# Optimization experiments

Measured on AMD Instinct MI355X. Metric: run time of the kernel, lower is better.

Reference implementation:

```python
import jax, jax.numpy as jnp
import numpy as np

HEADS, DIM_HEAD, DIM = 8, 64, 512
INNER = HEADS * DIM_HEAD  # 512


def setup_inputs() -> dict:
    key = jax.random.key(0)
    k1, k2, k3 = jax.random.split(key, 3)
    b, n = 2, 2048
    x = jax.random.normal(k1, (b, n, DIM), dtype=jnp.float32)
    # to_qkv: Linear(dim, 4*inner_dim, bias=False); weight stored [out, in]
    w_qkv = jax.random.normal(k2, (4 * INNER, DIM), dtype=jnp.float32) * (1.0 / np.sqrt(DIM))
    # to_out: Linear(2*inner_dim, dim) with bias
    w_out = jax.random.normal(k3, (DIM, 2 * INNER), dtype=jnp.float32) * (1.0 / np.sqrt(2 * INNER))
    b_out = jnp.zeros((DIM,), dtype=jnp.float32)
    return {"x": x, "w_qkv": w_qkv, "w_out": w_out, "b_out": b_out}


def reference(x, w_qkv, w_out, b_out):
    b, n, d = x.shape
    qkvt = x @ w_qkv.T  # [b, n, 4*inner]
    q, k, v, t = jnp.split(qkvt, 4, axis=-1)

    def split_heads(z):
        return z.reshape(b, n, HEADS, DIM_HEAD).transpose(0, 2, 1, 3)  # [b,h,n,dh]

    q, k, v, t = map(split_heads, (q, k, v, t))

    scale = DIM_HEAD ** -0.5
    dots = jnp.einsum('bhid,bhjd->bhij', q, k) * scale
    attn1 = jax.nn.softmax(dots, axis=-1)

    # fixed positional-decay attention: exp(-|i-j|/e), torch broadcast-normalized
    idx = jnp.arange(1, n + 1, dtype=x.dtype)  # linspace(1, n, n)
    tg = jnp.abs(idx[None, :] - idx[:, None])  # [n, n]
    a2 = jnp.exp(-tg / jnp.exp(jnp.asarray(1.0, x.dtype)))
    a2 = a2 / a2.sum(-1)  # broadcasts over last axis, as in the torch code

    out1 = jnp.einsum('bhij,bhjd->bhid', attn1, v)
    out2 = jnp.einsum('ij,bhjd->bhid', a2, t)
    out = jnp.concatenate([out1, out2], axis=-1)  # [b,h,n,2*dh]
    out = out.transpose(0, 2, 1, 3).reshape(b, n, HEADS * 2 * DIM_HEAD)  # [b,n,2*inner]
    return out @ w_out.T + b_out
```

## Files before the change

### kernel.cpp

```cpp
#include <hip/hip_runtime.h>
#include <hip/hip_bf16.h>
#include <stdint.h>

typedef unsigned short u16;
typedef __bf16 bf16;
typedef __bf16 bf16x8 __attribute__((ext_vector_type(8)));
typedef float f32x4 __attribute__((ext_vector_type(4)));
typedef float f32x16 __attribute__((ext_vector_type(16)));

#define NSEQ 2048
#define NDH 64
#define NH 8
#define QKS 2097152ull

__device__ __forceinline__ float b2f(u16 u) {
  union { float f; uint32_t i; } x; x.i = ((uint32_t)u) << 16; return x.f;
}
__device__ __forceinline__ u16 f2b(float f) {
  union { float f; uint32_t i; } x; x.f = f;
  const uint32_t r = x.i + 0x7FFFu + ((x.i >> 16) & 1u);
  return (u16)(r >> 16);
}
__device__ __forceinline__ uint32_t b2pk(float a, float b) {
  union { __hip_bfloat162 h; uint32_t u; } x;
  x.h = __float22bfloat162_rn(make_float2(a, b));
  return x.u;
}

__global__ __launch_bounds__(256) void k_gemm_qkvt(
    const float* __restrict__ X, const float* __restrict__ W, u16* __restrict__ qkvt) {
  __shared__ __align__(16) bf16 smem[18432];
  bf16* As = smem;
  bf16* Bs = smem + 5120;
  const int tid = threadIdx.x;
  const int n0 = blockIdx.x * 128;
  const int m0 = blockIdx.y * 128;
  const int w = tid >> 6, lane = tid & 63;
  const int wy = w >> 1, wx = w & 1;
  const int quad = lane >> 4, l15 = lane & 15;
  const int srow = tid >> 1, shalf = (tid & 1) * 16;
  const float* ax = X + (size_t)(m0 + srow) * 512 + shalf;
  const float* bx = W + (size_t)(n0 + srow) * 512 + shalf;
  f32x4 acc[4][4];
#pragma unroll
  for (int mt = 0; mt < 4; ++mt)
#pragma unroll
    for (int nt = 0; nt < 4; ++nt) acc[mt][nt] = (f32x4){0.f, 0.f, 0.f, 0.f};
  float4 af[4], bf4[4];
#pragma unroll
  for (int p = 0; p < 4; ++p) {
    af[p]  = *(const float4*)(ax + p * 4);
    bf4[p] = *(const float4*)(bx + p * 4);
  }
  for (int kc = 0; kc < 512; kc += 32) {
    __syncthreads();
    {
      uint4 ta = {b2pk(af[0].x, af[0].y), b2pk(af[0].z, af[0].w),
                  b2pk(af[1].x, af[1].y), b2pk(af[1].z, af[1].w)};
      uint4 tb = {b2pk(af[2].x, af[2].y), b2pk(af[2].z, af[2].w),
                  b2pk(af[3].x, af[3].y), b2pk(af[3].z, af[3].w)};
      *(uint4*)&As[srow * 40 + shalf]     = ta;
      *(uint4*)&As[srow * 40 + shalf + 8] = tb;
      uint4 tc = {b2pk(bf4[0].x, bf4[0].y), b2pk(bf4[0].z, bf4[0].w),
                  b2pk(bf4[1].x, bf4[1].y), b2pk(bf4[1].z, bf4[1].w)};
      uint4 td = {b2pk(bf4[2].x, bf4[2].y), b2pk(bf4[2].z, bf4[2].w),
                  b2pk(bf4[3].x, bf4[3].y), b2pk(bf4[3].z, bf4[3].w)};
      *(uint4*)&Bs[srow * 40 + shalf]     = tc;
      *(uint4*)&Bs[srow * 40 + shalf + 8] = td;
    }
    __syncthreads();
    if (kc + 32 < 512) {
#pragma unroll
      for (int p = 0; p < 4; ++p) {
        af[p]  = *(const float4*)(ax + kc + 32 + p * 4);
        bf4[p] = *(const float4*)(bx + kc + 32 + p * 4);
      }
    }
    bf16x8 afr[4], bfr[4];
#pragma unroll
    for (int mt = 0; mt < 4; ++mt)
      afr[mt] = *(const bf16x8*)&As[(wy * 64 + mt * 16 + l15) * 40 + quad * 8];
#pragma unroll
    for (int nt = 0; nt < 4; ++nt)
      bfr[nt] = *(const bf16x8*)&Bs[(wx * 64 + nt * 16 + l15) * 40 + quad * 8];
#pragma unroll
    for (int mt = 0; mt < 4; ++mt)
#pragma unroll
      for (int nt = 0; nt < 4; ++nt)
        acc[mt][nt] = __builtin_amdgcn_mfma_f32_16x16x32_bf16(afr[mt], bfr[nt], acc[mt][nt], 0, 0, 0);
  }
  __syncthreads();
  const int cbase = n0 + wx * 64;
  const int which = cbase >> 9;
  const int h     = (cbase >> 6) & 7;
  const float scale = (which == 0) ? 0.18033688011112043f : 1.0f;
  bf16* Cw = smem + w * 4608;
  if (which == 2) {
#pragma unroll
    for (int nt = 0; nt < 4; ++nt)
#pragma unroll
      for (int mt = 0; mt < 4; ++mt)
#pragma unroll
        for (int r = 0; r < 4; ++r)
          Cw[(nt * 16 + l15) * 72 + mt * 16 + quad * 4 + r] = (bf16)acc[mt][nt][r];
  } else {
#pragma unroll
    for (int mt = 0; mt < 4; ++mt)
#pragma unroll
      for (int nt = 0; nt < 4; ++nt)
#pragma unroll
        for (int r = 0; r < 4; ++r)
          Cw[(mt * 16 + quad * 4 + r) * 72 + nt * 16 + l15] = (bf16)(acc[mt][nt][r] * scale);
  }
  const int mb = m0 + wy * 64;
  const int bb = mb >> 11;
  const int nn0 = mb & (NSEQ - 1);
  if (which == 2) {
    u16* vt = qkvt + 2ull * QKS + (size_t)(bb * NH + h) * NDH * NSEQ;
#pragma unroll
    for (int p = 0; p < 8; ++p) {
      const int d = p * 8 + (lane >> 3);
      const int t8 = (lane & 7) * 8;
      const uint4 v = *(const uint4*)&Cw[d * 72 + t8];
      *(uint4*)(vt + (size_t)d * NSEQ + nn0 + t8) = v;
    }
  } else {
    u16* dst = qkvt + (size_t)which * QKS + ((size_t)(bb * NH + h) * NSEQ + nn0) * NDH;
#pragma unroll
    for (int p = 0; p < 8; ++p) {
      const int tok = p * 8 + (lane >> 3);
      const int c8 = (lane & 7) * 8;
      const uint4 v = *(const uint4*)&Cw[tok * 72 + c8];
      *(uint4*)(dst + (size_t)tok * NDH + c8) = v;
    }
  }
}

__global__ __launch_bounds__(256) void k_attn(
    const u16* __restrict__ qkvt, u16* __restrict__ out12) {
  __shared__ __align__(16) bf16 Qs[64 * 72];
  __shared__ __align__(16) bf16 KV[2 * 64 * 72];
  __shared__ __align__(16) bf16 Pw[4 * 32 * 72];
  __shared__ float Lpart[4][32];
  bf16* Ks = KV;
  bf16* Vt = KV + 64 * 72;
  const int tid = threadIdx.x;
  const int bh  = blockIdx.x;
  const int q0  = blockIdx.y * 64;
  const size_t base  = (size_t)bh * (NSEQ * NDH);
  const size_t vbase = 2ull * QKS + (size_t)bh * (NDH * NSEQ);
  const int wq = tid >> 6, lane = tid & 63;
  const int qh = wq >> 1, kh = wq & 1;
  const int l31 = lane & 31, hi = lane >> 5;
  const int srow = tid >> 2, sc0 = (tid & 3) * 16;
  {
    const u16* qp = qkvt + base + (size_t)(q0 + srow) * NDH + sc0;
    *(uint4*)&Qs[srow * 72 + sc0]     = *(const uint4*)qp;
    *(uint4*)&Qs[srow * 72 + sc0 + 8] = *(const uint4*)(qp + 8);
  }
  __syncthreads();
  bf16x8 qb[4];
#pragma unroll
  for (int c = 0; c < 4; ++c)
    qb[c] = *(const bf16x8*)&Qs[(qh * 32 + l31) * 72 + c * 16 + hi * 8];
  float lacc = 0.f;
  f32x16 o[2];
#pragma unroll
  for (int nt = 0; nt < 2; ++nt)
#pragma unroll
    for (int r = 0; r < 16; ++r) o[nt][r] = 0.f;
  const u16* kp = qkvt + QKS + base + (size_t)srow * NDH + sc0;
  const u16* vp = qkvt + vbase + (size_t)srow * NSEQ + sc0;
  uint4 k0 = *(const uint4*)kp;
  uint4 k1 = *(const uint4*)(kp + 8);
  uint4 v0 = *(const uint4*)vp;
  uint4 v1 = *(const uint4*)(vp + 8);
  for (int kt = 0; kt < 32; ++kt) {
    __syncthreads();
    *(uint4*)&Ks[srow * 72 + sc0]     = k0;
    *(uint4*)&Ks[srow * 72 + sc0 + 8] = k1;
    *(uint4*)&Vt[srow * 72 + sc0]     = v0;
    *(uint4*)&Vt[srow * 72 + sc0 + 8] = v1;
    __syncthreads();
    if (kt < 31) {
      const u16* kn = kp + (size_t)(kt + 1) * 64 * NDH;
      const u16* vn = vp + (kt + 1) * 64;
      k0 = *(const uint4*)kn;
      k1 = *(const uint4*)(kn + 8);
      v0 = *(const uint4*)vn;
      v1 = *(const uint4*)(vn + 8);
    }
    f32x16 s;
#pragma unroll
    for (int r = 0; r < 16; ++r) s[r] = 0.f;
#pragma unroll
    for (int c = 0; c < 4; ++c) {
      const bf16x8 ka = *(const bf16x8*)&Ks[(kh * 32 + l31) * 72 + c * 16 + hi * 8];
      s = __builtin_amdgcn_mfma_f32_32x32x16_bf16(ka, qb[c], s, 0, 0, 0);
    }
    float ts = 0.f;
#pragma unroll
    for (int r = 0; r < 16; ++r) {
      s[r] = __builtin_amdgcn_exp2f(s[r]);
      ts += s[r];
    }
    ts += __shfl_xor(ts, 32);
    lacc += ts;
    bf16* pr = Pw + (wq * 32 + l31) * 72;
#pragma unroll
    for (int g = 0; g < 4; ++g) {
      bf16 pk[4] = {(bf16)s[4 * g], (bf16)s[4 * g + 1],
                    (bf16)s[4 * g + 2], (bf16)s[4 * g + 3]};
      *(uint2*)&pr[g * 8 + hi * 4] = *(const uint2*)pk;
    }
#pragma unroll
    for (int c = 0; c < 2; ++c) {
      const bf16x8 pa = *(const bf16x8*)&Pw[(wq * 32 + l31) * 72 + c * 16 + hi * 8];
      const bf16x8 vb0 = *(const bf16x8*)&Vt[l31 * 72 + kh * 32 + c * 16 + hi * 8];
      const bf16x8 vb1 = *(const bf16x8*)&Vt[(32 + l31) * 72 + kh * 32 + c * 16 + hi * 8];
      o[0] = __builtin_amdgcn_mfma_f32_32x32x16_bf16(pa, vb0, o[0], 0, 0, 0);
      o[1] = __builtin_amdgcn_mfma_f32_32x32x16_bf16(pa, vb1, o[1], 0, 0, 0);
    }
  }
  __syncthreads();
  if (lane < 32) Lpart[wq][lane] = lacc;
  float* Osum = (float*)KV;
  if (kh == 1) {
#pragma unroll
    for (int nt = 0; nt < 2; ++nt)
#pragma unroll
      for (int r = 0; r < 16; ++r) {
        const int row = (r & 3) + 8 * (r >> 2) + 4 * hi;
        Osum[(qh * 32 + row) * 64 + nt * 32 + l31] = o[nt][r];
      }
  }
  __syncthreads();
  if (kh == 0) {
    const int bb = bh >> 3, h = bh & 7;
#pragma unroll
    for (int r = 0; r < 16; ++r) {
      const int row = (r & 3) + 8 * (r >> 2) + 4 * hi;
      const float lt = Lpart[qh * 2][row] + Lpart[qh * 2 + 1][row];
      const float inv = 1.f / lt;
      const int nn = q0 + qh * 32 + row;
      u16* dst = out12 + (size_t)(bb * NSEQ + nn) * 1024 + h * 128;
      dst[l31]      = f2b((o[0][r] + Osum[(qh * 32 + row) * 64 + l31]) * inv);
      dst[32 + l31] = f2b((o[1][r] + Osum[(qh * 32 + row) * 64 + 32 + l31]) * inv);
    }
  }
}

__global__ __launch_bounds__(256) void k_band(
    const u16* __restrict__ qkvt, u16* __restrict__ out12) {
  __shared__ float sinv[4][192];
  __shared__ float fbuf[4][64][68];
  const int tid = threadIdx.x;
  const int w = tid >> 6, d = tid & 63;
  const int c  = blockIdx.x * 4 + w;
  const int i0 = c * 64;
  const int bh = blockIdx.y;
  const size_t tb = 3ull * QKS + (size_t)bh * (NSEQ * NDH);
  const float EI = 0.36787944117144233f;
  const float RR = 0.69220062755534635f;
  const float OMR = 1.f - RR;
#pragma unroll
  for (int p = 0; p < 3; ++p) {
    const int j = i0 - 64 + p * 64 + d;
    const float r1 = __expf(-(float)(j + 1) * EI);
    const float r2 = __expf(-(float)(NSEQ - j) * EI);
    sinv[w][p * 64 + d] = OMR / (1.f - r1 + RR - r2);
  }
  const u16* tp = qkvt + tb + d;
  float f = 0.f;
  if (c > 0) {
#pragma unroll 8
    for (int jj = 0; jj < 64; ++jj)
      f = RR * f + sinv[w][jj] * b2f(tp[(size_t)(i0 - 64 + jj) * NDH]);
  }
#pragma unroll 8
  for (int jj = 0; jj < 64; ++jj) {
    f = RR * f + sinv[w][64 + jj] * b2f(tp[(size_t)(i0 + jj) * NDH]);
    fbuf[w][jj][d] = f;
  }
  float b = 0.f;
  if (c < 31) {
#pragma unroll 8
    for (int jj = 63; jj >= 0; --jj)
      b = RR * b + sinv[w][128 + jj] * b2f(tp[(size_t)(i0 + 64 + jj) * NDH]);
  }
  const int bb = bh >> 3, h = bh & 7;
#pragma unroll 8
  for (int jj = 63; jj >= 0; --jj) {
    const float g = sinv[w][64 + jj] * b2f(tp[(size_t)(i0 + jj) * NDH]);
    b = RR * b + g;
    out12[(size_t)(bb * NSEQ + i0 + jj) * 1024 + h * 128 + 64 + d] =
        f2b(fbuf[w][jj][d] + b - g);
  }
}

__global__ __launch_bounds__(256) void k_gemm_out(
    const u16* __restrict__ A, const float* __restrict__ W,
    const float* __restrict__ bias, float* __restrict__ out) {
  __shared__ __align__(16) float smemf[4352];
  bf16* As = (bf16*)smemf;
  bf16* Bs = (bf16*)smemf + 2560;
  const int tid = threadIdx.x;
  const int n0 = blockIdx.x * 64;
  const int m0 = blockIdx.y * 64;
  const int w = tid >> 6, lane = tid & 63;
  const int quad = lane >> 4, l15 = lane & 15;
  const int srow = tid >> 2, scol = (tid & 3) * 8;
  const u16*   ap = A + (size_t)(m0 + srow) * 1024 + scol;
  const float* bp = W + (size_t)(n0 + srow) * 1024 + scol;
  f32x4 acc[4];
#pragma unroll
  for (int nt = 0; nt < 4; ++nt) acc[nt] = (f32x4){0.f, 0.f, 0.f, 0.f};
  uint4 a0 = *(const uint4*)ap;
  float4 b0 = *(const float4*)bp;
  float4 b1 = *(const float4*)(bp + 4);
  for (int kc = 0; kc < 1024; kc += 32) {
    __syncthreads();
    *(uint4*)&As[srow * 40 + scol] = a0;
    {
      uint4 tb = {b2pk(b0.x, b0.y), b2pk(b0.z, b0.w),
                  b2pk(b1.x, b1.y), b2pk(b1.z, b1.w)};
      *(uint4*)&Bs[srow * 40 + scol] = tb;
    }
    __syncthreads();
    if (kc + 32 < 1024) {
      a0 = *(const uint4*)(ap + kc + 32);
      b0 = *(const float4*)(bp + kc + 32);
      b1 = *(const float4*)(bp + kc + 36);
    }
    const bf16x8 af = *(const bf16x8*)&As[(w * 16 + l15) * 40 + quad * 8];
#pragma unroll
    for (int nt = 0; nt < 4; ++nt) {
      const bf16x8 bfr = *(const bf16x8*)&Bs[(nt * 16 + l15) * 40 + quad * 8];
      acc[nt] = __builtin_amdgcn_mfma_f32_16x16x32_bf16(af, bfr, acc[nt], 0, 0, 0);
    }
  }
  float bias_v[4];
#pragma unroll
  for (int nt = 0; nt < 4; ++nt) bias_v[nt] = bias[n0 + nt * 16 + l15];
  __syncthreads();
  float* Cw = smemf + w * 1088;
#pragma unroll
  for (int nt = 0; nt < 4; ++nt)
#pragma unroll
    for (int r = 0; r < 4; ++r)
      Cw[(quad * 4 + r) * 68 + nt * 16 + l15] = acc[nt][r] + bias_v[nt];
#pragma unroll
  for (int p = 0; p < 4; ++p) {
    const int row = p * 4 + (lane >> 4);
    const int c4  = (lane & 15) * 4;
    const float4 v = *(const float4*)&Cw[row * 68 + c4];
    *(float4*)(out + (size_t)(m0 + w * 16 + row) * 512 + n0 + c4) = v;
  }
}

extern "C" void kernel_launch(void* const* d_in, const int* in_sizes, int n_in,
                              void* d_out, int out_size, void* d_ws, size_t ws_size,
                              hipStream_t stream) {
  (void)in_sizes; (void)n_in; (void)out_size; (void)ws_size;
  const float* x     = (const float*)d_in[0];
  const float* w_qkv = (const float*)d_in[1];
  const float* w_out = (const float*)d_in[2];
  const float* b_out = (const float*)d_in[3];
  float* out = (float*)d_out;
  u16* qkvt  = (u16*)d_ws;
  u16* out12 = (u16*)d_ws + 8ull * 1024 * 1024;
  k_gemm_qkvt<<<dim3(16, 32), 256, 0, stream>>>(x, w_qkv, qkvt);
  k_attn     <<<dim3(16, 32), 256, 0, stream>>>(qkvt, out12);
  k_band     <<<dim3(8, 16), 256, 0, stream>>>(qkvt, out12);
  k_gemm_out <<<dim3(8, 64), 256, 0, stream>>>(out12, w_out, b_out, out);
}
```

Before: 147.7 us.

## Pre-convert inputs to bf16 and stage GEMM tiles via direct global-to-LDS loads

Adds a conversion kernel that turns x, w_qkv and w_out into bf16 in workspace. Both GEMMs then load tiles with global_load_lds straight into unpadded shared memory instead of loading fp32 into registers and converting. The output GEMM also moves to a 64-wide K step with two sub-tiles per iteration. This trades an extra launch and a conversion pass for less register traffic, fewer conversions and fewer barriers. It also drops register prefetch overlap, and the unpadded 32-element row stride may cause LDS bank conflicts.

Result: faster. 142.4 us (-3.7%).

```diff
diff --git a/kernel.cpp b/kernel.cpp
--- a/kernel.cpp
+++ b/kernel.cpp
@@ -26,63 +26,65 @@
   x.h = __float22bfloat162_rn(make_float2(a, b));
   return x.u;
 }
+__device__ __forceinline__ void gl16(const void* g, void* l) {
+  __builtin_amdgcn_global_load_lds(
+      (const __attribute__((address_space(1))) void*)g,
+      (__attribute__((address_space(3))) void*)l, 16, 0, 0);
+}
+
+__global__ __launch_bounds__(256) void k_cvt(
+    const float* __restrict__ X, const float* __restrict__ Wq,
+    const float* __restrict__ Wo, u16* __restrict__ Xb,
+    u16* __restrict__ Wqb, u16* __restrict__ Wob) {
+  const int b = blockIdx.x;
+  const float* src; u16* dst; int idx;
+  if (b < 1024)      { src = X;  dst = Xb;  idx = b; }
+  else if (b < 1536) { src = Wq; dst = Wqb; idx = b - 1024; }
+  else               { src = Wo; dst = Wob; idx = b - 1536; }
+  const size_t off = ((size_t)idx * 256 + threadIdx.x) * 8;
+  const float4 a = *(const float4*)(src + off);
+  const float4 c = *(const float4*)(src + off + 4);
+  uint4 o = {b2pk(a.x, a.y), b2pk(a.z, a.w), b2pk(c.x, c.y), b2pk(c.z, c.w)};
+  *(uint4*)(dst + off) = o;
+}
 
 __global__ __launch_bounds__(256) void k_gemm_qkvt(
-    const float* __restrict__ X, const float* __restrict__ W, u16* __restrict__ qkvt) {
+    const u16* __restrict__ Xb, const u16* __restrict__ Wb, u16* __restrict__ qkvt) {
   __shared__ __align__(16) bf16 smem[18432];
   bf16* As = smem;
-  bf16* Bs = smem + 5120;
+  bf16* Bs = smem + 4096;
   const int tid = threadIdx.x;
   const int n0 = blockIdx.x * 128;
   const int m0 = blockIdx.y * 128;
   const int w = tid >> 6, lane = tid & 63;
   const int wy = w >> 1, wx = w & 1;
   const int quad = lane >> 4, l15 = lane & 15;
-  const int srow = tid >> 1, shalf = (tid & 1) * 16;
-  const float* ax = X + (size_t)(m0 + srow) * 512 + shalf;
-  const float* bx = W + (size_t)(n0 + srow) * 512 + shalf;
+  const int srow = tid >> 2, sc8 = (tid & 3) * 8;
+  const u16* ag = Xb + (size_t)(m0 + srow) * 512 + sc8;
+  const u16* bg = Wb + (size_t)(n0 + srow) * 512 + sc8;
+  char* aL0 = (char*)As + w * 1024;
+  char* aL1 = (char*)As + 4096 + w * 1024;
+  char* bL0 = (char*)Bs + w * 1024;
+  char* bL1 = (char*)Bs + 4096 + w * 1024;
   f32x4 acc[4][4];
 #pragma unroll
   for (int mt = 0; mt < 4; ++mt)
 #pragma unroll
     for (int nt = 0; nt < 4; ++nt) acc[mt][nt] = (f32x4){0.f, 0.f, 0.f, 0.f};
-  float4 af[4], bf4[4];
-#pragma unroll
-  for (int p = 0; p < 4; ++p) {
-    af[p]  = *(const float4*)(ax + p * 4);
-    bf4[p] = *(const float4*)(bx + p * 4);
-  }
   for (int kc = 0; kc < 512; kc += 32) {
     __syncthreads();
-    {
-      uint4 ta = {b2pk(af[0].x, af[0].y), b2pk(af[0].z, af[0].w),
-                  b2pk(af[1].x, af[1].y), b2pk(af[1].z, af[1].w)};
-      uint4 tb = {b2pk(af[2].x, af[2].y), b2pk(af[2].z, af[2].w),
-                  b2pk(af[3].x, af[3].y), b2pk(af[3].z, af[3].w)};
-      *(uint4*)&As[srow * 40 + shalf]     = ta;
-      *(uint4*)&As[srow * 40 + shalf + 8] = tb;
-      uint4 tc = {b2pk(bf4[0].x, bf4[0].y), b2pk(bf4[0].z, bf4[0].w),
-                  b2pk(bf4[1].x, bf4[1].y), b2pk(bf4[1].z, bf4[1].w)};
-      uint4 td = {b2pk(bf4[2].x, bf4[2].y), b2pk(bf4[2].z, bf4[2].w),
-                  b2pk(bf4[3].x, bf4[3].y), b2pk(bf4[3].z, bf4[3].w)};
-      *(uint4*)&Bs[srow * 40 + shalf]     = tc;
-      *(uint4*)&Bs[srow * 40 + shalf + 8] = td;
-    }
-    __syncthreads();
-    if (kc + 32 < 512) {
-#pragma unroll
-      for (int p = 0; p < 4; ++p) {
-        af[p]  = *(const float4*)(ax + kc + 32 + p * 4);
-        bf4[p] = *(const float4*)(bx + kc + 32 + p * 4);
-      }
-    }
+    gl16(ag + kc,            aL0);
+    gl16(ag + kc + 64 * 512, aL1);
+    gl16(bg + kc,            bL0);
+    gl16(bg + kc + 64 * 512, bL1);
+    __syncthreads();
     bf16x8 afr[4], bfr[4];
 #pragma unroll
     for (int mt = 0; mt < 4; ++mt)
-      afr[mt] = *(const bf16x8*)&As[(wy * 64 + mt * 16 + l15) * 40 + quad * 8];
+      afr[mt] = *(const bf16x8*)&As[(wy * 64 + mt * 16 + l15) * 32 + quad * 8];
 #pragma unroll
     for (int nt = 0; nt < 4; ++nt)
-      bfr[nt] = *(const bf16x8*)&Bs[(wx * 64 + nt * 16 + l15) * 40 + quad * 8];
+      bfr[nt] = *(const bf16x8*)&Bs[(wx * 64 + nt * 16 + l15) * 32 + quad * 8];
 #pragma unroll
     for (int mt = 0; mt < 4; ++mt)
 #pragma unroll
@@ -299,44 +301,43 @@
 }
 
 __global__ __launch_bounds__(256) void k_gemm_out(
-    const u16* __restrict__ A, const float* __restrict__ W,
+    const u16* __restrict__ A, const u16* __restrict__ Wb,
     const float* __restrict__ bias, float* __restrict__ out) {
   __shared__ __align__(16) float smemf[4352];
-  bf16* As = (bf16*)smemf;
-  bf16* Bs = (bf16*)smemf + 2560;
+  bf16* As0 = (bf16*)smemf;
+  bf16* As1 = (bf16*)smemf + 2048;
+  bf16* Bs0 = (bf16*)smemf + 4096;
+  bf16* Bs1 = (bf16*)smemf + 6144;
   const int tid = threadIdx.x;
   const int n0 = blockIdx.x * 64;
   const int m0 = blockIdx.y * 64;
   const int w = tid >> 6, lane = tid & 63;
   const int quad = lane >> 4, l15 = lane & 15;
-  const int srow = tid >> 2, scol = (tid & 3) * 8;
-  const u16*   ap = A + (size_t)(m0 + srow) * 1024 + scol;
-  const float* bp = W + (size_t)(n0 + srow) * 1024 + scol;
+  const int srow = tid >> 2, sc8 = (tid & 3) * 8;
+  const u16* ap = A  + (size_t)(m0 + srow) * 1024 + sc8;
+  const u16* bp = Wb + (size_t)(n0 + srow) * 1024 + sc8;
+  char* aL0 = (char*)smemf + w * 1024;
+  char* aL1 = (char*)smemf + 4096  + w * 1024;
+  char* bL0 = (char*)smemf + 8192  + w * 1024;
+  char* bL1 = (char*)smemf + 12288 + w * 1024;
   f32x4 acc[4];
 #pragma unroll
   for (int nt = 0; nt < 4; ++nt) acc[nt] = (f32x4){0.f, 0.f, 0.f, 0.f};
-  uint4 a0 = *(const uint4*)ap;
-  float4 b0 = *(const float4*)bp;
-  float4 b1 = *(const float4*)(bp + 4);
-  for (int kc = 0; kc < 1024; kc += 32) {
-    __syncthreads();
-    *(uint4*)&As[srow * 40 + scol] = a0;
-    {
-      uint4 tb = {b2pk(b0.x, b0.y), b2pk(b0.z, b0.w),
-                  b2pk(b1.x, b1.y), b2pk(b1.z, b1.w)};
-      *(uint4*)&Bs[srow * 40 + scol] = tb;
-    }
-    __syncthreads();
-    if (kc + 32 < 1024) {
-      a0 = *(const uint4*)(ap + kc + 32);
-      b0 = *(const float4*)(bp + kc + 32);
-      b1 = *(const float4*)(bp + kc + 36);
-    }
-    const bf16x8 af = *(const bf16x8*)&As[(w * 16 + l15) * 40 + quad * 8];
+  for (int kc = 0; kc < 1024; kc += 64) {
+    __syncthreads();
+    gl16(ap + kc,      aL0);
+    gl16(ap + kc + 32, aL1);
+    gl16(bp + kc,      bL0);
+    gl16(bp + kc + 32, bL1);
+    __syncthreads();
+    const int fr = (w * 16 + l15) * 32 + quad * 8;
+    const bf16x8 af0 = *(const bf16x8*)&As0[fr];
+    const bf16x8 af1 = *(const bf16x8*)&As1[fr];
 #pragma unroll
     for (int nt = 0; nt < 4; ++nt) {
-      const bf16x8 bfr = *(const bf16x8*)&Bs[(nt * 16 + l15) * 40 + quad * 8];
-      acc[nt] = __builtin_amdgcn_mfma_f32_16x16x32_bf16(af, bfr, acc[nt], 0, 0, 0);
+      const int br = (nt * 16 + l15) * 32 + quad * 8;
+      acc[nt] = __builtin_amdgcn_mfma_f32_16x16x32_bf16(af0, *(const bf16x8*)&Bs0[br], acc[nt], 0, 0, 0);
+      acc[nt] = __builtin_amdgcn_mfma_f32_16x16x32_bf16(af1, *(const bf16x8*)&Bs1[br], acc[nt], 0, 0, 0);
     }
   }
   float bias_v[4];
@@ -367,10 +368,15 @@
   const float* w_out = (const float*)d_in[2];
   const float* b_out = (const float*)d_in[3];
   float* out = (float*)d_out;
-  u16* qkvt  = (u16*)d_ws;
-  u16* out12 = (u16*)d_ws + 8ull * 1024 * 1024;
-  k_gemm_qkvt<<<dim3(16, 32), 256, 0, stream>>>(x, w_qkv, qkvt);
+  u16* ws    = (u16*)d_ws;
+  u16* qkvt  = ws;
+  u16* out12 = ws + 8ull  * 1024 * 1024;
+  u16* Xb    = ws + 12ull * 1024 * 1024;
+  u16* Wqb   = ws + 14ull * 1024 * 1024;
+  u16* Wob   = ws + 15ull * 1024 * 1024;
+  k_cvt      <<<dim3(1792), 256, 0, stream>>>(x, w_qkv, w_out, Xb, Wqb, Wob);
+  k_gemm_qkvt<<<dim3(16, 32), 256, 0, stream>>>(Xb, Wqb, qkvt);
   k_attn     <<<dim3(16, 32), 256, 0, stream>>>(qkvt, out12);
   k_band     <<<dim3(8, 16), 256, 0, stream>>>(qkvt, out12);
-  k_gemm_out <<<dim3(8, 64), 256, 0, stream>>>(out12, w_out, b_out, out);
-}
+  k_gemm_out <<<dim3(8, 64), 256, 0, stream>>>(out12, Wob, b_out, out);
+}
```
